# Kernel tuning notes

Hardware: AMD Instinct MI355X
Metric: run time of the kernel (lower is better)

## Reference

```python
import jax, jax.numpy as jnp
import numpy as np

N, E = 50000, 400000
IN_DIM = OUT_DIM = 128
T, R, H = 4, 8, 8
DK = OUT_DIM // H


def setup_inputs() -> dict:
    key = jax.random.key(0)
    ks = jax.random.split(key, 20)
    xav = lambda k, i, o: jax.random.uniform(k, (T, i, o), jnp.float32, -1.0, 1.0) * np.sqrt(6.0 / (i + o))
    return {
        "node_inp": jax.random.normal(ks[0], (N, IN_DIM), jnp.float32),
        "node_type": jax.random.randint(ks[1], (N,), 0, T),
        "edge_index": jax.random.randint(ks[2], (2, E), 0, N),
        "edge_type": jax.random.randint(ks[3], (E,), 0, R),
        "edge_sign": jax.random.randint(ks[4], (E,), 0, 3) - 1,  # values in {-1,0,1}
        "Wq": xav(ks[5], IN_DIM, OUT_DIM), "bq": jnp.zeros((T, OUT_DIM)),
        "Wk": xav(ks[6], IN_DIM, OUT_DIM), "bk": jnp.zeros((T, OUT_DIM)),
        "Wv": xav(ks[7], IN_DIM, OUT_DIM), "bv": jnp.zeros((T, OUT_DIM)),
        "rel_q": jax.random.normal(ks[8], (R, H, DK), jnp.float32),
        "rel_k": jax.random.normal(ks[9], (R, H, DK), jnp.float32),
        "rel_v": jax.random.normal(ks[10], (R, H, DK), jnp.float32),
        "sign_k_neutral": jnp.ones((H, DK), jnp.float32),
        "sign_v_neutral": jnp.ones((H, DK), jnp.float32),
        "rel_bias": jnp.zeros((R, H), jnp.float32),
        "skip": jnp.ones((T,), jnp.float32),
        "ln_gamma": jnp.ones((T, OUT_DIM), jnp.float32),
        "ln_beta": jnp.zeros((T, OUT_DIM), jnp.float32),
    }


def reference(node_inp, node_type, edge_index, edge_type, edge_sign,
              Wq, bq, Wk, bk, Wv, bv, rel_q, rel_k, rel_v,
              sign_k_neutral, sign_v_neutral, rel_bias, skip, ln_gamma, ln_beta):
    n = node_inp.shape[0]
    src, dst = edge_index[0], edge_index[1]
    rows = jnp.arange(n)
    # per-node-type linear projections: compute for all types, select by node_type
    proj = lambda W, b: (jnp.einsum('ni,tio->tno', node_inp, W) + b[:, None, :])[node_type, rows]
    Q = proj(Wq, bq).reshape(n, H, DK)
    K = proj(Wk, bk).reshape(n, H, DK)
    V = proj(Wv, bv).reshape(n, H, DK)
    # sign tables: [neg(-1), pos(+1), neutral]
    ones = jnp.ones((H, DK), node_inp.dtype)
    sign_k_all = jnp.stack([-ones, ones, sign_k_neutral], 0)
    sign_v_all = jnp.stack([-ones, ones, sign_v_neutral], 0)
    s_idx = jnp.where(edge_sign == -1, 0, jnp.where(edge_sign == 1, 1, 2))
    q_eff = Q[dst] * rel_q[edge_type]                      # [E,H,DK]
    k_eff = K[src] * rel_k[edge_type] * sign_k_all[s_idx]
    v_eff = V[src] * rel_v[edge_type] * sign_v_all[s_idx]
    scores = (q_eff * k_eff).sum(-1) / np.sqrt(DK) + rel_bias[edge_type]  # [E,H]
    # segment softmax over dst groups
    smax = jax.ops.segment_max(scores, dst, num_segments=n)
    ex = jnp.exp(scores - smax[dst])
    ssum = jax.ops.segment_sum(ex, dst, num_segments=n)
    attn = ex / (ssum[dst] + 1e-16)
    msg = (v_eff * attn[..., None]).reshape(-1, OUT_DIM)
    out = jnp.zeros((n, OUT_DIM), node_inp.dtype).at[dst].add(msg)
    # per-type gated skip + layernorm
    alpha = jax.nn.sigmoid(skip)[node_type][:, None]
    pre = alpha * out + (1.0 - alpha) * node_inp
    mu = pre.mean(-1, keepdims=True)
    var = ((pre - mu) ** 2).mean(-1, keepdims=True)
    normed = (pre - mu) / jnp.sqrt(var + 1e-5)
    return normed * ln_gamma[node_type] + ln_beta[node_type]
```

## Files before the change

### kernel.cpp

```cpp
#include <hip/hip_runtime.h>
#include <hip/hip_bf16.h>


#define D 128
#define NT 4
#define NR 8
#define NH 8
#define SCAN_BS 256

__global__ void k_hist(const int* __restrict__ nt, const int* __restrict__ ei,
                       int N, int E, int* __restrict__ tcnt, int* __restrict__ deg) {
    __shared__ int lcnt[NT];
    int tid = threadIdx.x;
    if (tid < NT) lcnt[tid] = 0;
    __syncthreads();
    int g = blockIdx.x * 256 + tid;
    if (g < N) atomicAdd(&lcnt[nt[g]], 1);
    if (g < E) atomicAdd(&deg[ei[E + g]], 1);
    __syncthreads();
    if (tid < NT && lcnt[tid]) atomicAdd(&tcnt[tid], lcnt[tid]);
}

__global__ __launch_bounds__(SCAN_BS) void k_scan1(const int* __restrict__ deg, int N,
                                                   int* __restrict__ bsum) {
    __shared__ int lds[SCAN_BS];
    int ti = threadIdx.x;
    int i = blockIdx.x * SCAN_BS + ti;
    lds[ti] = (i < N) ? deg[i] : 0;
    __syncthreads();
    for (int off = SCAN_BS >> 1; off > 0; off >>= 1) {
        if (ti < off) lds[ti] += lds[ti + off];
        __syncthreads();
    }
    if (ti == 0) bsum[blockIdx.x] = lds[0];
}

__global__ __launch_bounds__(SCAN_BS) void k_scan2(const int* __restrict__ bsum, int NB,
                                                   const int* __restrict__ tcnt,
                                                   int* __restrict__ bbase,
                                                   int* __restrict__ toff,
                                                   int* __restrict__ row_ptr, int N, int E) {
    __shared__ int lds[SCAN_BS];
    int ti = threadIdx.x;
    int v = (ti < NB) ? bsum[ti] : 0;
    lds[ti] = v;
    __syncthreads();
    for (int off = 1; off < SCAN_BS; off <<= 1) {
        int t = (ti >= off) ? lds[ti - off] : 0;
        __syncthreads();
        lds[ti] += t;
        __syncthreads();
    }
    if (ti < NB) bbase[ti] = lds[ti] - v;
    if (ti == 0) {
        int a = 0;
        for (int t = 0; t < NT; t++) { toff[t] = a; a += tcnt[t]; }
        toff[NT] = a;
        row_ptr[N] = E;
    }
}

__global__ __launch_bounds__(SCAN_BS) void k_scan3(const int* __restrict__ deg, int N,
                                                   const int* __restrict__ bbase,
                                                   int* __restrict__ row_ptr,
                                                   int* __restrict__ ecur) {
    __shared__ int lds[SCAN_BS];
    int ti = threadIdx.x;
    int i = blockIdx.x * SCAN_BS + ti;
    int v = (i < N) ? deg[i] : 0;
    lds[ti] = v;
    __syncthreads();
    for (int off = 1; off < SCAN_BS; off <<= 1) {
        int t = (ti >= off) ? lds[ti - off] : 0;
        __syncthreads();
        lds[ti] += t;
        __syncthreads();
    }
    if (i < N) {
        int ex = bbase[blockIdx.x] + lds[ti] - v;
        row_ptr[i] = ex;
        ecur[i] = ex;
    }
}

__global__ void k_scatter(const int* __restrict__ nt, const int* __restrict__ ei,
                          const int* __restrict__ et, const int* __restrict__ es,
                          int N, int E, int* __restrict__ tcur,
                          const int* __restrict__ toff, int* __restrict__ sorted,
                          int* __restrict__ ecur, int* __restrict__ csr_rec) {
    __shared__ int lcnt[NT];
    __shared__ int lbase[NT];
    int tid = threadIdx.x;
    if (tid < NT) lcnt[tid] = 0;
    __syncthreads();
    int g = blockIdx.x * 256 + tid;
    int t = -1, myrank = 0;
    if (g < N) {
        t = nt[g];
        myrank = atomicAdd(&lcnt[t], 1);
    }
    __syncthreads();
    if (tid < NT) lbase[tid] = lcnt[tid] ? atomicAdd(&tcur[tid], lcnt[tid]) : 0;
    __syncthreads();
    if (t >= 0) sorted[toff[t] + lbase[t] + myrank] = g;

    if (g < E) {
        int src = ei[g];
        int d = ei[E + g];
        int r = et[g];
        int sg = es[g];
        int p = atomicAdd(&ecur[d], 1);
        csr_rec[p] = src | (r << 17) | ((sg + 1) << 20);
    }
}

__global__ __launch_bounds__(512, 4) void k_proj(
    const float* __restrict__ x, const int* __restrict__ sorted,
    const int* __restrict__ toff,
    const float* __restrict__ Wq, const float* __restrict__ bq,
    const float* __restrict__ Wk, const float* __restrict__ bk,
    const float* __restrict__ Wv, const float* __restrict__ bv,
    float* __restrict__ Q, float* __restrict__ K, float* __restrict__ V) {
    __shared__ float xs[128 * 129];
    __shared__ int sid[128];
    int tid = threadIdx.x;
    int b = blockIdx.x;
    int t = -1, p0 = 0;
    int cum = 0;
    for (int tt = 0; tt < NT; tt++) {
        int cnt_t = toff[tt + 1] - toff[tt];
        int nb = (cnt_t + 127) >> 7;
        if (t < 0 && b < cum + nb) { t = tt; p0 = toff[tt] + (b - cum) * 128; }
        cum += nb;
    }
    if (t < 0) return;
    int cnt = min(128, toff[t + 1] - p0);

    if (tid < 128) sid[tid] = (tid < cnt) ? sorted[p0 + tid] : -1;
    __syncthreads();
    for (int j = 0; j < 8; j++) {
        int idx = j * 512 + tid;
        int row = idx >> 5, c4 = (idx & 31) * 4;
        int node = sid[row];
        if (node >= 0) {
            float4 v = *(const float4*)(x + (size_t)node * D + c4);
            float* p = &xs[row * 129 + c4];
            p[0] = v.x; p[1] = v.y; p[2] = v.z; p[3] = v.w;
        }
    }
    __syncthreads();

    int og = tid & 15, ng = tid >> 4;
    int o0 = og * 8;
    int m = blockIdx.y;
    const float* Wm = (m == 0) ? Wq : (m == 1) ? Wk : Wv;
    const float* bm = (m == 0) ? bq : (m == 1) ? bk : bv;
    float* Om = (m == 0) ? Q : (m == 1) ? K : V;
    Wm += (size_t)t * D * D;
    bm += t * D;

    float acc[4][8];
    float bias[8];
#pragma unroll
    for (int c = 0; c < 8; c++) bias[c] = bm[o0 + c];
#pragma unroll
    for (int r = 0; r < 4; r++)
#pragma unroll
        for (int c = 0; c < 8; c++) acc[r][c] = bias[c];

#pragma unroll 4
    for (int k = 0; k < D; k++) {
        float4 w0 = *(const float4*)(Wm + k * D + o0);
        float4 w1 = *(const float4*)(Wm + k * D + o0 + 4);
        float w8[8] = {w0.x, w0.y, w0.z, w0.w, w1.x, w1.y, w1.z, w1.w};
        float xv[4];
#pragma unroll
        for (int r = 0; r < 4; r++) xv[r] = xs[(ng * 4 + r) * 129 + k];
#pragma unroll
        for (int r = 0; r < 4; r++)
#pragma unroll
            for (int c = 0; c < 8; c++) acc[r][c] += xv[r] * w8[c];
    }
#pragma unroll
    for (int r = 0; r < 4; r++) {
        int node = sid[ng * 4 + r];
        if (node < 0) continue;
        float4 a0 = {acc[r][0], acc[r][1], acc[r][2], acc[r][3]};
        float4 a1 = {acc[r][4], acc[r][5], acc[r][6], acc[r][7]};
        *(float4*)(Om + (size_t)node * D + o0) = a0;
        *(float4*)(Om + (size_t)node * D + o0 + 4) = a1;
    }
}

__global__ __launch_bounds__(256) void k_agg(
    const int* __restrict__ row_ptr, const int* __restrict__ csr_rec,
    const int* __restrict__ nt, const float* __restrict__ x,
    const float* __restrict__ Qt, const float* __restrict__ Kt,
    const float* __restrict__ Vt, const float* __restrict__ rq,
    const float* __restrict__ rk, const float* __restrict__ rv,
    const float* __restrict__ skn, const float* __restrict__ svn,
    const float* __restrict__ rb, const float* __restrict__ skip,
    const float* __restrict__ gamma, const float* __restrict__ beta,
    float* __restrict__ out, int N) {
    __shared__ float l_rq[NR * 132];
    __shared__ float l_rk[NR * 132];
    __shared__ float l_rv[NR * 132];
    __shared__ float l_rb[NR * NH];
    int tid = threadIdx.x;
    for (int idx = tid; idx < NR * D; idx += 256) {
        int r = idx >> 7, c = idx & 127;
        l_rq[r * 132 + c] = rq[idx];
        l_rk[r * 132 + c] = rk[idx];
        l_rv[r * 132 + c] = rv[idx];
    }
    if (tid < NR * NH) l_rb[tid] = rb[tid];
    __syncthreads();

    int wid = (blockIdx.x * 256 + tid) >> 6;
    if (wid >= N) return;
    int lane = tid & 63;
    int h = lane >> 3, li = lane & 7;
    int d0 = lane * 2;
    int dst = wid;
    int rp0 = row_ptr[dst];
    int deg = row_ptr[dst + 1] - rp0;

    float4 q4[4], sk4[4];
#pragma unroll
    for (int j = 0; j < 4; j++) {
        q4[j] = *(const float4*)(Qt + (size_t)dst * D + h * 16 + 4 * j);
        sk4[j] = *(const float4*)(skn + h * 16 + 4 * j);
    }
    float2 sv2 = *(const float2*)(svn + d0);
    float2 xi = *(const float2*)(x + (size_t)dst * D + d0);
    int t = nt[dst];

    float m = -INFINITY, lsum = 0.f, acc0 = 0.f, acc1 = 0.f;

    for (int c0 = 0; c0 < deg; c0 += 8) {
        int cn = min(8, deg - c0);
        bool valid = li < cn;
        int recA = csr_rec[rp0 + c0 + (valid ? li : 0)];
        int srcA = recA & 0x1FFFF;
        int rA = (recA >> 17) & 7;
        int sgA = ((recA >> 20) & 3) - 1;
        bool neuA = (sgA == 0);
        float fsgA = (float)sgA;
        const float* kp = Kt + (size_t)srcA * D + h * 16;
        const float* rqp = &l_rq[rA * 132 + h * 16];
        const float* rkp = &l_rk[rA * 132 + h * 16];
        float dot = 0.f;
#pragma unroll
        for (int j = 0; j < 4; j++) {
            float4 k4 = *(const float4*)(kp + 4 * j);
            float4 a4 = *(const float4*)(rqp + 4 * j);
            float4 b4 = *(const float4*)(rkp + 4 * j);
            float f0 = neuA ? sk4[j].x : fsgA;
            float f1 = neuA ? sk4[j].y : fsgA;
            float f2 = neuA ? sk4[j].z : fsgA;
            float f3 = neuA ? sk4[j].w : fsgA;
            dot += q4[j].x * a4.x * k4.x * b4.x * f0;
            dot += q4[j].y * a4.y * k4.y * b4.y * f1;
            dot += q4[j].z * a4.z * k4.z * b4.z * f2;
            dot += q4[j].w * a4.w * k4.w * b4.w * f3;
        }
        float scA = valid ? dot * 0.25f + l_rb[rA * NH + h] : -INFINITY;
        float cm = scA;
        cm = fmaxf(cm, __shfl_xor(cm, 1));
        cm = fmaxf(cm, __shfl_xor(cm, 2));
        cm = fmaxf(cm, __shfl_xor(cm, 4));
        float nm = fmaxf(m, cm);
        float resc = __expf(m - nm);
        acc0 *= resc; acc1 *= resc; lsum *= resc;
        m = nm;
        int rec_[8];
        float w_[8];
        float2 v2_[8];
#pragma unroll
        for (int i = 0; i < 8; i++) {
            rec_[i] = __shfl(recA, i);
            int src = rec_[i] & 0x1FFFF;
            v2_[i] = *(const float2*)(Vt + (size_t)src * D + d0);
            float s = __shfl(scA, (lane & 56) | i);
            w_[i] = __expf(s - m);
        }
#pragma unroll
        for (int i = 0; i < 8; i++) {
            float w = w_[i];
            lsum += w;
            int r = (rec_[i] >> 17) & 7;
            int sg = ((rec_[i] >> 20) & 3) - 1;
            float2 r2 = *(const float2*)(&l_rv[r * 132 + d0]);
            bool neu = (sg == 0);
            float f0 = neu ? sv2.x : (float)sg;
            float f1 = neu ? sv2.y : (float)sg;
            acc0 += w * v2_[i].x * r2.x * f0;
            acc1 += w * v2_[i].y * r2.y * f1;
        }
    }
    float winv = 1.f / (lsum + 1e-16f);
    float a0 = acc0 * winv, a1 = acc1 * winv;

    float alpha = 1.f / (1.f + __expf(-skip[t]));
    float p0 = alpha * a0 + (1.f - alpha) * xi.x;
    float p1 = alpha * a1 + (1.f - alpha) * xi.y;
    float rs = p0 + p1, rsq = p0 * p0 + p1 * p1;
#pragma unroll
    for (int o = 1; o < 64; o <<= 1) {
        rs += __shfl_xor(rs, o);
        rsq += __shfl_xor(rsq, o);
    }
    float mu = rs * (1.f / 128.f);
    float var = rsq * (1.f / 128.f) - mu * mu;
    float rstd = rsqrtf(var + 1e-5f);
    float2 g2 = *(const float2*)(gamma + t * D + d0);
    float2 b2 = *(const float2*)(beta + t * D + d0);
    float o0 = (p0 - mu) * rstd * g2.x + b2.x;
    float o1 = (p1 - mu) * rstd * g2.y + b2.y;
    *(float2*)(out + (size_t)dst * D + d0) = make_float2(o0, o1);
}

extern "C" void kernel_launch(void* const* d_in, const int* in_sizes, int n_in,
                              void* d_out, int out_size, void* d_ws, size_t ws_size,
                              hipStream_t stream) {
    const float* x   = (const float*)d_in[0];
    const int*  nt   = (const int*)d_in[1];
    const int*  ei   = (const int*)d_in[2];
    const int*  et   = (const int*)d_in[3];
    const int*  es   = (const int*)d_in[4];
    const float* Wq  = (const float*)d_in[5];
    const float* bq  = (const float*)d_in[6];
    const float* Wk  = (const float*)d_in[7];
    const float* bk  = (const float*)d_in[8];
    const float* Wv  = (const float*)d_in[9];
    const float* bv  = (const float*)d_in[10];
    const float* rq  = (const float*)d_in[11];
    const float* rk  = (const float*)d_in[12];
    const float* rv  = (const float*)d_in[13];
    const float* skn = (const float*)d_in[14];
    const float* svn = (const float*)d_in[15];
    const float* rb  = (const float*)d_in[16];
    const float* skp = (const float*)d_in[17];
    const float* gma = (const float*)d_in[18];
    const float* bta = (const float*)d_in[19];
    float* out = (float*)d_out;

    int N = in_sizes[0] / D;
    int E = in_sizes[2] / 2;
    int NB = (N + SCAN_BS - 1) / SCAN_BS;

    float* Q = (float*)d_ws;
    float* K = Q + (size_t)N * D;
    float* V = K + (size_t)N * D;
    int* deg     = (int*)(V + (size_t)N * D);
    int* tcnt    = deg + N;
    int* tcur    = tcnt + NT;
    int* row_ptr = tcur + NT;
    int* ecur    = row_ptr + N + 1;
    int* toff    = ecur + N;
    int* sorted  = toff + 8;
    int* csr_rec = sorted + N;
    int* bsum    = csr_rec + E;
    int* bbase   = bsum + NB;

    hipMemsetAsync(deg, 0, (size_t)(N + 2 * NT) * sizeof(int), stream);

    int gbNE = (max(N, E) + 255) / 256;
    k_hist<<<gbNE, 256, 0, stream>>>(nt, ei, N, E, tcnt, deg);
    k_scan1<<<NB, SCAN_BS, 0, stream>>>(deg, N, bsum);
    k_scan2<<<1, SCAN_BS, 0, stream>>>(bsum, NB, tcnt, bbase, toff, row_ptr, N, E);
    k_scan3<<<NB, SCAN_BS, 0, stream>>>(deg, N, bbase, row_ptr, ecur);
    k_scatter<<<gbNE, 256, 0, stream>>>(nt, ei, et, es, N, E, tcur, toff, sorted,
                                        ecur, csr_rec);
    int nbp = (N + 127) / 128 + NT;
    k_proj<<<dim3(nbp, 3), 512, 0, stream>>>(x, sorted, toff, Wq, bq, Wk, bk,
                                             Wv, bv, Q, K, V);
    k_agg<<<(N * 64 + 255) / 256, 256, 0, stream>>>(row_ptr, csr_rec, nt, x, Q, K, V,
                                                    rq, rk, rv, skn, svn, rb, skp,
                                                    gma, bta, out, N);
}
```

Before: 353.0 us.

## Store K and V projections as bf16 and split hist/scatter kernels

K and V are written by the projection kernel as bf16 with round-to-nearest-even and unpacked to fp32 in the aggregation kernel. This halves the bytes of the per-edge random gathers of K and V rows. The combined node/edge histogram and scatter kernels are also split into separate node and edge kernels, which adds launches but removes the oversized combined grids. It adds bf16 rounding error to attention scores and messages.

```diff
diff --git a/kernel.cpp b/kernel.cpp
--- a/kernel.cpp
+++ b/kernel.cpp
@@ -8,17 +8,31 @@
 #define NH 8
 #define SCAN_BS 256
 
-__global__ void k_hist(const int* __restrict__ nt, const int* __restrict__ ei,
-                       int N, int E, int* __restrict__ tcnt, int* __restrict__ deg) {
+typedef unsigned short ushort_t;
+typedef unsigned int uint_t;
+
+static __device__ __forceinline__ ushort_t f2bf(float f) {
+    uint_t u = __float_as_uint(f);
+    return (ushort_t)((u + 0x7FFFu + ((u >> 16) & 1u)) >> 16);
+}
+static __device__ __forceinline__ float bf2f(ushort_t h) {
+    return __uint_as_float(((uint_t)h) << 16);
+}
+
+__global__ void k_hist_n(const int* __restrict__ nt, int N, int* __restrict__ tcnt) {
     __shared__ int lcnt[NT];
     int tid = threadIdx.x;
     if (tid < NT) lcnt[tid] = 0;
     __syncthreads();
     int g = blockIdx.x * 256 + tid;
     if (g < N) atomicAdd(&lcnt[nt[g]], 1);
+    __syncthreads();
+    if (tid < NT && lcnt[tid]) atomicAdd(&tcnt[tid], lcnt[tid]);
+}
+
+__global__ void k_hist_e(const int* __restrict__ ei, int E, int* __restrict__ deg) {
+    int g = blockIdx.x * 256 + threadIdx.x;
     if (g < E) atomicAdd(&deg[ei[E + g]], 1);
-    __syncthreads();
-    if (tid < NT && lcnt[tid]) atomicAdd(&tcnt[tid], lcnt[tid]);
 }
 
 __global__ __launch_bounds__(SCAN_BS) void k_scan1(const int* __restrict__ deg, int N,
@@ -83,11 +97,8 @@
     }
 }
 
-__global__ void k_scatter(const int* __restrict__ nt, const int* __restrict__ ei,
-                          const int* __restrict__ et, const int* __restrict__ es,
-                          int N, int E, int* __restrict__ tcur,
-                          const int* __restrict__ toff, int* __restrict__ sorted,
-                          int* __restrict__ ecur, int* __restrict__ csr_rec) {
+__global__ void k_scat_n(const int* __restrict__ nt, int N, int* __restrict__ tcur,
+                         const int* __restrict__ toff, int* __restrict__ sorted) {
     __shared__ int lcnt[NT];
     __shared__ int lbase[NT];
     int tid = threadIdx.x;
@@ -103,7 +114,12 @@
     if (tid < NT) lbase[tid] = lcnt[tid] ? atomicAdd(&tcur[tid], lcnt[tid]) : 0;
     __syncthreads();
     if (t >= 0) sorted[toff[t] + lbase[t] + myrank] = g;
-
+}
+
+__global__ void k_scat_e(const int* __restrict__ ei, const int* __restrict__ et,
+                         const int* __restrict__ es, int E,
+                         int* __restrict__ ecur, int* __restrict__ csr_rec) {
+    int g = blockIdx.x * 256 + threadIdx.x;
     if (g < E) {
         int src = ei[g];
         int d = ei[E + g];
@@ -120,7 +136,7 @@
     const float* __restrict__ Wq, const float* __restrict__ bq,
     const float* __restrict__ Wk, const float* __restrict__ bk,
     const float* __restrict__ Wv, const float* __restrict__ bv,
-    float* __restrict__ Q, float* __restrict__ K, float* __restrict__ V) {
+    float* __restrict__ Q, ushort_t* __restrict__ Kb, ushort_t* __restrict__ Vb) {
     __shared__ float xs[128 * 129];
     __shared__ int sid[128];
     int tid = threadIdx.x;
@@ -155,7 +171,6 @@
     int m = blockIdx.y;
     const float* Wm = (m == 0) ? Wq : (m == 1) ? Wk : Wv;
     const float* bm = (m == 0) ? bq : (m == 1) ? bk : bv;
-    float* Om = (m == 0) ? Q : (m == 1) ? K : V;
     Wm += (size_t)t * D * D;
     bm += t * D;
 
@@ -185,18 +200,28 @@
     for (int r = 0; r < 4; r++) {
         int node = sid[ng * 4 + r];
         if (node < 0) continue;
-        float4 a0 = {acc[r][0], acc[r][1], acc[r][2], acc[r][3]};
-        float4 a1 = {acc[r][4], acc[r][5], acc[r][6], acc[r][7]};
-        *(float4*)(Om + (size_t)node * D + o0) = a0;
-        *(float4*)(Om + (size_t)node * D + o0 + 4) = a1;
+        if (m == 0) {
+            float4 a0 = {acc[r][0], acc[r][1], acc[r][2], acc[r][3]};
+            float4 a1 = {acc[r][4], acc[r][5], acc[r][6], acc[r][7]};
+            *(float4*)(Q + (size_t)node * D + o0) = a0;
+            *(float4*)(Q + (size_t)node * D + o0 + 4) = a1;
+        } else {
+            ushort_t* Om = (m == 1) ? Kb : Vb;
+            uint_t p[4];
+#pragma unroll
+            for (int c = 0; c < 4; c++)
+                p[c] = (uint_t)f2bf(acc[r][2 * c]) | ((uint_t)f2bf(acc[r][2 * c + 1]) << 16);
+            uint4 pk = {p[0], p[1], p[2], p[3]};
+            *(uint4*)(Om + (size_t)node * D + o0) = pk;
+        }
     }
 }
 
 __global__ __launch_bounds__(256) void k_agg(
     const int* __restrict__ row_ptr, const int* __restrict__ csr_rec,
     const int* __restrict__ nt, const float* __restrict__ x,
-    const float* __restrict__ Qt, const float* __restrict__ Kt,
-    const float* __restrict__ Vt, const float* __restrict__ rq,
+    const float* __restrict__ Qt, const ushort_t* __restrict__ Kb,
+    const ushort_t* __restrict__ Vb, const float* __restrict__ rq,
     const float* __restrict__ rk, const float* __restrict__ rv,
     const float* __restrict__ skn, const float* __restrict__ svn,
     const float* __restrict__ rb, const float* __restrict__ skip,
@@ -246,23 +271,24 @@
         int sgA = ((recA >> 20) & 3) - 1;
         bool neuA = (sgA == 0);
         float fsgA = (float)sgA;
-        const float* kp = Kt + (size_t)srcA * D + h * 16;
+        const ushort_t* kp = Kb + (size_t)srcA * D + h * 16;
         const float* rqp = &l_rq[rA * 132 + h * 16];
         const float* rkp = &l_rk[rA * 132 + h * 16];
         float dot = 0.f;
 #pragma unroll
         for (int j = 0; j < 4; j++) {
-            float4 k4 = *(const float4*)(kp + 4 * j);
+            ushort4 kk = ((const ushort4*)kp)[j];
+            float k0 = bf2f(kk.x), k1 = bf2f(kk.y), k2 = bf2f(kk.z), k3 = bf2f(kk.w);
             float4 a4 = *(const float4*)(rqp + 4 * j);
             float4 b4 = *(const float4*)(rkp + 4 * j);
             float f0 = neuA ? sk4[j].x : fsgA;
             float f1 = neuA ? sk4[j].y : fsgA;
             float f2 = neuA ? sk4[j].z : fsgA;
             float f3 = neuA ? sk4[j].w : fsgA;
-            dot += q4[j].x * a4.x * k4.x * b4.x * f0;
-            dot += q4[j].y * a4.y * k4.y * b4.y * f1;
-            dot += q4[j].z * a4.z * k4.z * b4.z * f2;
-            dot += q4[j].w * a4.w * k4.w * b4.w * f3;
+            dot += q4[j].x * a4.x * k0 * b4.x * f0;
+            dot += q4[j].y * a4.y * k1 * b4.y * f1;
+            dot += q4[j].z * a4.z * k2 * b4.z * f2;
+            dot += q4[j].w * a4.w * k3 * b4.w * f3;
         }
         float scA = valid ? dot * 0.25f + l_rb[rA * NH + h] : -INFINITY;
         float cm = scA;
@@ -275,12 +301,12 @@
         m = nm;
         int rec_[8];
         float w_[8];
-        float2 v2_[8];
+        uint_t v2_[8];
 #pragma unroll
         for (int i = 0; i < 8; i++) {
             rec_[i] = __shfl(recA, i);
             int src = rec_[i] & 0x1FFFF;
-            v2_[i] = *(const float2*)(Vt + (size_t)src * D + d0);
+            v2_[i] = *(const uint_t*)(Vb + (size_t)src * D + d0);
             float s = __shfl(scA, (lane & 56) | i);
             w_[i] = __expf(s - m);
         }
@@ -290,12 +316,14 @@
             lsum += w;
             int r = (rec_[i] >> 17) & 7;
             int sg = ((rec_[i] >> 20) & 3) - 1;
+            float v0 = bf2f((ushort_t)(v2_[i] & 0xFFFF));
+            float v1 = bf2f((ushort_t)(v2_[i] >> 16));
             float2 r2 = *(const float2*)(&l_rv[r * 132 + d0]);
             bool neu = (sg == 0);
             float f0 = neu ? sv2.x : (float)sg;
             float f1 = neu ? sv2.y : (float)sg;
-            acc0 += w * v2_[i].x * r2.x * f0;
-            acc1 += w * v2_[i].y * r2.y * f1;
+            acc0 += w * v0 * r2.x * f0;
+            acc1 += w * v1 * r2.y * f1;
         }
     }
     float winv = 1.f / (lsum + 1e-16f);
@@ -349,10 +377,10 @@
     int E = in_sizes[2] / 2;
     int NB = (N + SCAN_BS - 1) / SCAN_BS;
 
-    float* Q = (float*)d_ws;
-    float* K = Q + (size_t)N * D;
-    float* V = K + (size_t)N * D;
-    int* deg     = (int*)(V + (size_t)N * D);
+    float*    Q  = (float*)d_ws;
+    ushort_t* Kb = (ushort_t*)(Q + (size_t)N * D);
+    ushort_t* Vb = Kb + (size_t)N * D;
+    int* deg     = (int*)(Vb + (size_t)N * D);
     int* tcnt    = deg + N;
     int* tcur    = tcnt + NT;
     int* row_ptr = tcur + NT;
@@ -365,17 +393,19 @@
 
     hipMemsetAsync(deg, 0, (size_t)(N + 2 * NT) * sizeof(int), stream);
 
-    int gbNE = (max(N, E) + 255) / 256;
-    k_hist<<<gbNE, 256, 0, stream>>>(nt, ei, N, E, tcnt, deg);
+    int gbN = (N + 255) / 256;
+    int gbE = (E + 255) / 256;
+    k_hist_n<<<gbN, 256, 0, stream>>>(nt, N, tcnt);
+    k_hist_e<<<gbE, 256, 0, stream>>>(ei, E, deg);
     k_scan1<<<NB, SCAN_BS, 0, stream>>>(deg, N, bsum);
     k_scan2<<<1, SCAN_BS, 0, stream>>>(bsum, NB, tcnt, bbase, toff, row_ptr, N, E);
     k_scan3<<<NB, SCAN_BS, 0, stream>>>(deg, N, bbase, row_ptr, ecur);
-    k_scatter<<<gbNE, 256, 0, stream>>>(nt, ei, et, es, N, E, tcur, toff, sorted,
-                                        ecur, csr_rec);
+    k_scat_n<<<gbN, 256, 0, stream>>>(nt, N, tcur, toff, sorted);
+    k_scat_e<<<gbE, 256, 0, stream>>>(ei, et, es, E, ecur, csr_rec);
     int nbp = (N + 127) / 128 + NT;
     k_proj<<<dim3(nbp, 3), 512, 0, stream>>>(x, sorted, toff, Wq, bq, Wk, bk,
-                                             Wv, bv, Q, K, V);
-    k_agg<<<(N * 64 + 255) / 256, 256, 0, stream>>>(row_ptr, csr_rec, nt, x, Q, K, V,
+                                             Wv, bv, Q, Kb, Vb);
+    k_agg<<<(N * 64 + 255) / 256, 256, 0, stream>>>(row_ptr, csr_rec, nt, x, Q, Kb, Vb,
                                                     rq, rk, rv, skn, svn, rb, skp,
                                                     gma, bta, out, N);
 }
```

Result: faster. 340.4 us (-3.6%).
